# Performance work log

Hardware: AMD Instinct MI355X
Metric: run time of the kernel (lower is better)

The kernel has to match this reference:

```python
import jax, jax.numpy as jnp
import numpy as np

NUM_HEADS = 8
HEAD_SPLITS = [2, 3, 3]            # heads per crpe window {3:2, 5:3, 7:3}
WINDOWS = [3, 5, 7]


def dwconv(x, w, b, pad):
    """Depthwise conv. x: [B,C,H,W], w: [C,1,kh,kw] (OIHW), b: [C]."""
    y = jax.lax.conv_general_dilated(
        x, w, window_strides=(1, 1), padding=[(pad, pad), (pad, pad)],
        dimension_numbers=("NCHW", "OIHW", "NCHW"),
        feature_group_count=x.shape[1])
    return y + b[None, :, None, None]


def layernorm(x, w, b, eps=1e-6):
    m = jnp.mean(x, axis=-1, keepdims=True)
    v = jnp.mean(jnp.square(x - m), axis=-1, keepdims=True)
    return (x - m) * jax.lax.rsqrt(v + eps) * w + b


def setup_inputs() -> dict:
    key = jax.random.key(0)
    ks = jax.random.split(key, 16)
    B, Hs, Ws, C = 16, 56, 56, 512
    N = Hs * Ws
    Ch = C // NUM_HEADS
    hid = int(C * 4.0)

    def rn(k, shape, s=0.02):
        return jax.random.normal(k, shape, jnp.float32) * s

    return {
        "x": jax.random.normal(ks[0], (B, N, C), jnp.float32),
        "H": Hs, "W": Ws,
        "cpe_w": rn(ks[1], (C, 1, 3, 3)), "cpe_b": jnp.zeros((C,), jnp.float32),
        "ln1_w": jnp.ones((C,), jnp.float32), "ln1_b": jnp.zeros((C,), jnp.float32),
        "qkv_w": rn(ks[2], (C, 3 * C)),
        "proj_w": rn(ks[3], (C, C)), "proj_b": jnp.zeros((C,), jnp.float32),
        "w3": rn(ks[4], (HEAD_SPLITS[0] * Ch, 1, 3, 3)), "b3": jnp.zeros((HEAD_SPLITS[0] * Ch,), jnp.float32),
        "w5": rn(ks[5], (HEAD_SPLITS[1] * Ch, 1, 5, 5)), "b5": jnp.zeros((HEAD_SPLITS[1] * Ch,), jnp.float32),
        "w7": rn(ks[6], (HEAD_SPLITS[2] * Ch, 1, 7, 7)), "b7": jnp.zeros((HEAD_SPLITS[2] * Ch,), jnp.float32),
        "ln2_w": jnp.ones((C,), jnp.float32), "ln2_b": jnp.zeros((C,), jnp.float32),
        "fc1_w": rn(ks[7], (C, hid)), "fc1_b": jnp.zeros((hid,), jnp.float32),
        "fc2_w": rn(ks[8], (hid, C)), "fc2_b": jnp.zeros((C,), jnp.float32),
    }


def reference(x, H, W, cpe_w, cpe_b, ln1_w, ln1_b, qkv_w, proj_w, proj_b,
              w3, b3, w5, b5, w7, b7, ln2_w, ln2_b, fc1_w, fc1_b, fc2_w, fc2_b):
    B, N, C = x.shape
    h = NUM_HEADS
    Ch = C // h
    scale = Ch ** -0.5

    # --- ConvPosEnc (no cls token: N == H*W branch) ---
    feat = jnp.transpose(x, (0, 2, 1)).reshape(B, C, H, W)
    feat = dwconv(feat, cpe_w, cpe_b, pad=1) + feat
    x0 = jnp.transpose(feat.reshape(B, C, N), (0, 2, 1))  # [B,N,C]

    # --- FactorAttnConvRelPosEnc ---
    cur = layernorm(x0, ln1_w, ln1_b)
    qkv = (cur @ qkv_w).reshape(B, N, 3, h, Ch)
    qkv = jnp.transpose(qkv, (2, 0, 3, 1, 4))  # [3,B,h,N,Ch]
    q, k, v = qkv[0], qkv[1], qkv[2]

    k_sm = jax.nn.softmax(k, axis=2)                    # softmax over tokens
    kv = jnp.einsum("bhnk,bhnv->bhkv", k_sm, v)         # [B,h,Ch,Ch]
    factor_att = jnp.einsum("bhnk,bhkv->bhnv", q, kv)   # [B,h,N,Ch]

    # ConvRelPosEnc: grouped depthwise convs on v per head split
    v_img = jnp.transpose(v, (0, 1, 3, 2)).reshape(B, h * Ch, H, W)
    c0, c1 = HEAD_SPLITS[0] * Ch, (HEAD_SPLITS[0] + HEAD_SPLITS[1]) * Ch
    conv_v = jnp.concatenate([
        dwconv(v_img[:, :c0], w3, b3, pad=1),
        dwconv(v_img[:, c0:c1], w5, b5, pad=2),
        dwconv(v_img[:, c1:], w7, b7, pad=3),
    ], axis=1)
    conv_v = jnp.transpose(conv_v.reshape(B, h, Ch, N), (0, 1, 3, 2))  # [B,h,N,Ch]
    crpe = q * conv_v

    attn = scale * factor_att + crpe
    attn = jnp.transpose(attn, (0, 2, 1, 3)).reshape(B, N, C)
    attn = attn @ proj_w + proj_b

    x0 = x0 + attn

    # --- FFN ---
    cur = layernorm(x0, ln2_w, ln2_b)
    hdn = jax.nn.gelu(cur @ fc1_w + fc1_b, approximate=False)
    out = x0 + (hdn @ fc2_w + fc2_b)
    return out
```

## Files before the change

### kernel.cpp

```cpp
#include <hip/hip_runtime.h>
#include <hip/hip_bf16.h>

typedef unsigned short ushort_t;
typedef unsigned int uint_t;

typedef float f32x4 __attribute__((ext_vector_type(4)));
typedef short s16x8 __attribute__((ext_vector_type(8)));

#define HW 56
#define NTOK 3136
#define CDIM 512
#define NHEAD 8
#define CH 64
#define QKVC 1536
#define HID 2048
#define NSEG 28
#define SEGLEN 112

#define WPK_TOTAL 19976

__device__ __forceinline__ float b2f(ushort_t u) {
    union { uint_t i; float f; } cv; cv.i = ((uint_t)u) << 16; return cv.f;
}
__device__ __forceinline__ ushort_t f2b(float f) {
    union { __hip_bfloat16 h; ushort_t u; } cv; cv.h = __float2bfloat16(f); return cv.u;
}
__device__ __forceinline__ uint_t pk2(float a, float b) {
    return (uint_t)f2b(a) | ((uint_t)f2b(b) << 16);
}

__device__ __forceinline__ void gload_lds16(const ushort_t* g, ushort_t* l) {
    __builtin_amdgcn_global_load_lds(
        (const __attribute__((address_space(1))) void*)g,
        (__attribute__((address_space(3))) void*)l, 16, 0, 0);
}

__global__ __launch_bounds__(256) void k_transpose(const float* __restrict__ in,
                                                   ushort_t* __restrict__ out,
                                                   int K, int Npr) {
    __shared__ float tile[32][33];
    int tx = threadIdx.x & 31, ty = threadIdx.x >> 5;
    int kb = blockIdx.y * 32, nb = blockIdx.x * 32;
#pragma unroll
    for (int i = 0; i < 4; i++)
        tile[ty + i * 8][tx] = in[(size_t)(kb + ty + i * 8) * Npr + nb + tx];
    __syncthreads();
#pragma unroll
    for (int i = 0; i < 4; i++)
        out[(size_t)(nb + ty + i * 8) * K + kb + tx] = f2b(tile[tx][ty + i * 8]);
}

__global__ __launch_bounds__(256) void k_wtrans(const float* __restrict__ cpe_w,
                                                const float* __restrict__ w3,
                                                const float* __restrict__ w5,
                                                const float* __restrict__ w7,
                                                float* __restrict__ wpk) {
    int idx = blockIdx.x * 256 + threadIdx.x;
    if (idx < 4608) {
        int i = idx / 512, c = idx % 512;
        wpk[idx] = cpe_w[c * 9 + i];
    } else if (idx < 5760) {
        int r = idx - 4608; int i = r / 128, c = r % 128;
        wpk[idx] = w3[c * 9 + i];
    } else if (idx < 10560) {
        int r = idx - 5760; int i = r / 192, c = r % 192;
        wpk[idx] = w5[c * 25 + i];
    } else if (idx < 19968) {
        int r = idx - 10560; int i = r / 192, c = r % 192;
        wpk[idx] = w7[c * 49 + i];
    } else if (idx < WPK_TOTAL) {
        wpk[idx] = 0.f;
    }
}

__global__ __launch_bounds__(256) void k_cpe(const float* __restrict__ x,
                                             const float* __restrict__ wpk,
                                             const float* __restrict__ bias,
                                             float* __restrict__ x0) {
    int t = threadIdx.x;
    int tok = t >> 7;
    int c0 = (t & 127) * 4;
    int bb = blockIdx.y;
    int n = blockIdx.x * 2 + tok;
    int y = n / HW, xx = n % HW;
    const float* xb = x + ((size_t)bb * NTOK) * CDIM + c0;
    const float* zf = wpk + 19968;
    float4 a = *(const float4*)(bias + c0);
#pragma unroll
    for (int i = 0; i < 9; i++) {
        int ky = i / 3 - 1, kx = i % 3 - 1;
        int yy = y + ky, xc = xx + kx;
        bool ok = (unsigned)yy < HW && (unsigned)xc < HW;
        const float* ap = ok ? (xb + (size_t)(yy * HW + xc) * CDIM) : zf;
        float4 d = *(const float4*)ap;
        float4 w = *(const float4*)(wpk + i * 512 + c0);
        a.x += w.x * d.x; a.y += w.y * d.y; a.z += w.z * d.z; a.w += w.w * d.w;
    }
    float4 ctr = *(const float4*)(xb + (size_t)n * CDIM);
    a.x += ctr.x; a.y += ctr.y; a.z += ctr.z; a.w += ctr.w;
    *(float4*)(x0 + ((size_t)bb * NTOK + n) * CDIM + c0) = a;
}

__global__ __launch_bounds__(256) void k_ln(const float* __restrict__ in,
                                            const float* __restrict__ w,
                                            const float* __restrict__ b,
                                            ushort_t* __restrict__ out) {
    int wid = threadIdx.x >> 6, lane = threadIdx.x & 63;
    size_t row = (size_t)blockIdx.x * 4 + wid;
    const float* p = in + row * CDIM + lane * 8;
    float4 v0 = *(const float4*)p;
    float4 v1 = *(const float4*)(p + 4);
    float v[8] = { v0.x, v0.y, v0.z, v0.w, v1.x, v1.y, v1.z, v1.w };
    float s = 0.f, s2 = 0.f;
#pragma unroll
    for (int i = 0; i < 8; i++) { s += v[i]; s2 += v[i] * v[i]; }
#pragma unroll
    for (int m = 1; m < 64; m <<= 1) { s += __shfl_xor(s, m); s2 += __shfl_xor(s2, m); }
    float mean = s * (1.f / CDIM);
    float var = s2 * (1.f / CDIM) - mean * mean;
    float rstd = rsqrtf(var + 1e-6f);
    float4 w0 = *(const float4*)(w + lane * 8);
    float4 w1 = *(const float4*)(w + lane * 8 + 4);
    float4 b0 = *(const float4*)(b + lane * 8);
    float4 b1 = *(const float4*)(b + lane * 8 + 4);
    float wv[8] = { w0.x, w0.y, w0.z, w0.w, w1.x, w1.y, w1.z, w1.w };
    float bv[8] = { b0.x, b0.y, b0.z, b0.w, b1.x, b1.y, b1.z, b1.w };
    float o[8];
#pragma unroll
    for (int i = 0; i < 8; i++) o[i] = (v[i] - mean) * rstd * wv[i] + bv[i];
    uint4 ro;
    ro.x = pk2(o[0], o[1]); ro.y = pk2(o[2], o[3]); ro.z = pk2(o[4], o[5]); ro.w = pk2(o[6], o[7]);
    *(uint4*)(out + row * CDIM + lane * 8) = ro;
}

template <int EPI>
__global__ __launch_bounds__(256, 3) void k_gemm(const ushort_t* __restrict__ A,
                                                 const ushort_t* __restrict__ Bt,
                                                 const float* __restrict__ bias,
                                                 const float* __restrict__ res,
                                                 void* __restrict__ outv,
                                                 int M, int Npr, int K) {
    __shared__ ushort_t As[128 * 64];
    __shared__ ushort_t Bs[128 * 64];
    int t = threadIdx.x;
    int m0 = blockIdx.y * 128, n0 = blockIdx.x * 128;
    int wid = t >> 6, lane = t & 63, q = lane >> 4, r16 = lane & 15;
    int wr = wid >> 1, wc = wid & 1;
    f32x4 acc[4][4] = {};

    int srow = lane >> 3;
    int scol = ((lane & 7) ^ srow) * 8;
    const ushort_t* pA[4];
    const ushort_t* pB[4];
    int lofs[4];
#pragma unroll
    for (int c = 0; c < 4; c++) {
        int rowc = wid * 32 + c * 8 + srow;
        int ra = m0 + rowc; if (ra > M - 1) ra = M - 1;
        pA[c] = A + (size_t)ra * K + scol;
        pB[c] = Bt + (size_t)(n0 + rowc) * K + scol;
        lofs[c] = (wid * 32 + c * 8) * 64;
    }

    for (int k0 = 0; k0 < K; k0 += 64) {
#pragma unroll
        for (int c = 0; c < 4; c++) gload_lds16(pA[c] + k0, &As[lofs[c]]);
#pragma unroll
        for (int c = 0; c < 4; c++) gload_lds16(pB[c] + k0, &Bs[lofs[c]]);
        __syncthreads();
#pragma unroll
        for (int kk = 0; kk < 64; kk += 32) {
            s16x8 a[4], b[4];
#pragma unroll
            for (int i = 0; i < 4; i++) {
                int R = wr * 64 + i * 16 + r16;
                a[i] = *(const s16x8*)&As[R * 64 + ((kk + q * 8) ^ ((R & 7) * 8))];
            }
#pragma unroll
            for (int j = 0; j < 4; j++) {
                int S = wc * 64 + j * 16 + r16;
                b[j] = *(const s16x8*)&Bs[S * 64 + ((kk + q * 8) ^ ((S & 7) * 8))];
            }
#pragma unroll
            for (int mi = 0; mi < 4; mi++)
#pragma unroll
                for (int ni = 0; ni < 4; ni++)
                    acc[mi][ni] = __builtin_amdgcn_mfma_f32_16x16x32_bf16(a[mi], b[ni], acc[mi][ni], 0, 0, 0);
        }
        __syncthreads();
    }

#pragma unroll
    for (int mi = 0; mi < 4; mi++) {
#pragma unroll
        for (int ni = 0; ni < 4; ni++) {
            int col = n0 + wc * 64 + ni * 16 + r16;
            float bv = 0.f;
            if (EPI != 0) bv = bias[col];
#pragma unroll
            for (int r = 0; r < 4; r++) {
                int row = m0 + wr * 64 + mi * 16 + q * 4 + r;
                if (row >= M) continue;
                float xv = acc[mi][ni][r];
                size_t idx = (size_t)row * Npr + col;
                if (EPI == 0) {
                    ((ushort_t*)outv)[idx] = f2b(xv);
                } else if (EPI == 1) {
                    ((float*)outv)[idx] = xv + bv + res[idx];
                } else {
                    xv += bv;
                    xv = 0.5f * xv * (1.f + erff(xv * 0.70710678118654752f));
                    ((ushort_t*)outv)[idx] = f2b(xv);
                }
            }
        }
    }
}

__global__ __launch_bounds__(256) void k_sm_part(const ushort_t* __restrict__ qkv,
                                                 float* __restrict__ mxp,
                                                 float* __restrict__ ssp) {
    int cblk = blockIdx.x, seg = blockIdx.y, b = blockIdx.z;
    int ch = threadIdx.x & 63, nt = threadIdx.x >> 6;
    int c0 = cblk * 64;
    const ushort_t* base = qkv + (size_t)b * NTOK * QKVC + CDIM + c0 + ch;
    int nbeg = seg * SEGLEN, nend = nbeg + SEGLEN;
    __shared__ float red[4][64];
    float mx = -1e30f;
    for (int n = nbeg + nt; n < nend; n += 4) mx = fmaxf(mx, b2f(base[(size_t)n * QKVC]));
    red[nt][ch] = mx;
    __syncthreads();
    mx = fmaxf(fmaxf(red[0][ch], red[1][ch]), fmaxf(red[2][ch], red[3][ch]));
    __syncthreads();
    float s = 0.f;
    for (int n = nbeg + nt; n < nend; n += 4) s += __expf(b2f(base[(size_t)n * QKVC]) - mx);
    red[nt][ch] = s;
    __syncthreads();
    if (nt == 0) {
        s = red[0][ch] + red[1][ch] + red[2][ch] + red[3][ch];
        size_t o = ((size_t)b * CDIM + c0 + ch) * NSEG + seg;
        mxp[o] = mx;
        ssp[o] = s;
    }
}

__global__ __launch_bounds__(512) void k_sm_red(const float* __restrict__ mxp,
                                                const float* __restrict__ ssp,
                                                float* __restrict__ Mx,
                                                float* __restrict__ Sx) {
    int b = blockIdx.x, c = threadIdx.x;
    const float* mp = mxp + ((size_t)b * CDIM + c) * NSEG;
    const float* sp = ssp + ((size_t)b * CDIM + c) * NSEG;
    float m = -1e30f;
#pragma unroll 4
    for (int s = 0; s < NSEG; s++) m = fmaxf(m, mp[s]);
    float S = 0.f;
#pragma unroll 4
    for (int s = 0; s < NSEG; s++) S += sp[s] * __expf(mp[s] - m);
    Mx[b * CDIM + c] = m;
    Sx[b * CDIM + c] = S;
}

__global__ __launch_bounds__(256) void k_kv_part(const ushort_t* __restrict__ qkv,
                                                 const float* __restrict__ Mx,
                                                 float* __restrict__ kvpart) {
    int hd = blockIdx.x, seg = blockIdx.y, b = blockIdx.z;
    int c0 = hd * CH;
    int t = threadIdx.x, tx = t & 15, ty = t >> 4;
    __shared__ float mx[64];
    __shared__ float ek[8][64];
    __shared__ float vv[8][64];
    if (t < 64) mx[t] = Mx[b * CDIM + c0 + t];
    __syncthreads();
    float acc[4][4] = {};
    const ushort_t* kbase = qkv + (size_t)b * NTOK * QKVC + CDIM + c0;
    const ushort_t* vbase = kbase + CDIM;
    int nbeg = seg * SEGLEN;
    for (int n0 = nbeg; n0 < nbeg + SEGLEN; n0 += 8) {
        for (int idx = t; idx < 512; idx += 256) {
            int r = idx >> 6, ch = idx & 63;
            ek[r][ch] = __expf(b2f(kbase[(size_t)(n0 + r) * QKVC + ch]) - mx[ch]);
            vv[r][ch] = b2f(vbase[(size_t)(n0 + r) * QKVC + ch]);
        }
        __syncthreads();
#pragma unroll
        for (int r = 0; r < 8; r++) {
            float ekv[4], vvv[4];
#pragma unroll
            for (int i = 0; i < 4; i++) ekv[i] = ek[r][ty * 4 + i];
#pragma unroll
            for (int j = 0; j < 4; j++) vvv[j] = vv[r][tx * 4 + j];
#pragma unroll
            for (int i = 0; i < 4; i++)
#pragma unroll
                for (int j = 0; j < 4; j++) acc[i][j] += ekv[i] * vvv[j];
        }
        __syncthreads();
    }
    float* outp = kvpart + (((size_t)(b * NHEAD + hd)) * NSEG + seg) * 4096;
#pragma unroll
    for (int i = 0; i < 4; i++)
#pragma unroll
        for (int j = 0; j < 4; j++)
            outp[(size_t)(ty * 4 + i) * CH + tx * 4 + j] = acc[i][j];
}

__global__ __launch_bounds__(256) void k_kv_red(const float* __restrict__ kvpart,
                                                const float* __restrict__ Sx,
                                                float* __restrict__ kv) {
    int quad = blockIdx.x, hd = blockIdx.y, b = blockIdx.z;
    int bh = b * NHEAD + hd;
    int t = threadIdx.x;
    const float* basep = kvpart + ((size_t)bh * NSEG) * 4096 + quad * 1024;
    const float scale = 0.125f;
#pragma unroll
    for (int k = 0; k < 4; k++) {
        int e = k * 256 + t;
        float s = 0.f;
        for (int sg = 0; sg < NSEG; sg++) s += basep[(size_t)sg * 4096 + e];
        int ck = (quad * 1024 + e) >> 6;
        float sinv = scale / Sx[b * CDIM + hd * CH + ck];
        kv[(size_t)bh * 4096 + quad * 1024 + e] = s * sinv;
    }
}

__global__ __launch_bounds__(256) void k_convv(const ushort_t* __restrict__ qkv,
                                               const float* __restrict__ wpk,
                                               const float* __restrict__ b3,
                                               const float* __restrict__ b5,
                                               const float* __restrict__ b7,
                                               ushort_t* __restrict__ conv) {
    int t = threadIdx.x;
    int wv = t >> 6, lane = t & 63;
    int bb = blockIdx.y;
    int n0 = blockIdx.x * 16 + wv * 4;
    int ch0 = lane * 8;
    int ks, pad, base, stride; const float* bias;
    if (lane < 16)      { ks = 3; pad = 1; base = 4608 + ch0;          stride = 128; bias = b3 + ch0; }
    else if (lane < 40) { ks = 5; pad = 2; base = 5760 + (ch0 - 128);  stride = 192; bias = b5 + (ch0 - 128); }
    else                { ks = 7; pad = 3; base = 10560 + (ch0 - 320); stride = 192; bias = b7 + (ch0 - 320); }
    int ks2 = ks * ks;
    const ushort_t* vb = qkv + (size_t)bb * NTOK * QKVC + 2 * CDIM + ch0;
    const ushort_t* zp = (const ushort_t*)(wpk + 19968);
    float4 blo = *(const float4*)(bias);
    float4 bhi = *(const float4*)(bias + 4);
    float acc[4][8];
    int ty[4], txx[4];
#pragma unroll
    for (int k4 = 0; k4 < 4; k4++) {
        int n = n0 + k4; ty[k4] = n / HW; txx[k4] = n % HW;
        acc[k4][0] = blo.x; acc[k4][1] = blo.y; acc[k4][2] = blo.z; acc[k4][3] = blo.w;
        acc[k4][4] = bhi.x; acc[k4][5] = bhi.y; acc[k4][6] = bhi.z; acc[k4][7] = bhi.w;
    }
    int ky = -pad, kx = -pad;
    for (int i = 0; i < 49; i++) {
        bool act = i < ks2;
        int ie = act ? i : 0;
        const float* wp = wpk + base + ie * stride;
        float4 wlo = *(const float4*)wp;
        float4 whi = *(const float4*)(wp + 4);
        float w[8] = { wlo.x, wlo.y, wlo.z, wlo.w, whi.x, whi.y, whi.z, whi.w };
#pragma unroll
        for (int k4 = 0; k4 < 4; k4++) {
            int yy = ty[k4] + ky, xc = txx[k4] + kx;
            bool ok = act && (unsigned)yy < HW && (unsigned)xc < HW;
            const ushort_t* ap = ok ? (vb + (size_t)(yy * HW + xc) * QKVC) : zp;
            uint4 d = *(const uint4*)ap;
            float dv[8];
            dv[0] = b2f(d.x & 0xffff); dv[1] = b2f(d.x >> 16);
            dv[2] = b2f(d.y & 0xffff); dv[3] = b2f(d.y >> 16);
            dv[4] = b2f(d.z & 0xffff); dv[5] = b2f(d.z >> 16);
            dv[6] = b2f(d.w & 0xffff); dv[7] = b2f(d.w >> 16);
#pragma unroll
            for (int j = 0; j < 8; j++) acc[k4][j] += w[j] * dv[j];
        }
        kx++; if (kx > pad) { kx = -pad; ky++; }
    }
#pragma unroll
    for (int k4 = 0; k4 < 4; k4++) {
        int n = n0 + k4;
        uint4 o;
        o.x = pk2(acc[k4][0], acc[k4][1]);
        o.y = pk2(acc[k4][2], acc[k4][3]);
        o.z = pk2(acc[k4][4], acc[k4][5]);
        o.w = pk2(acc[k4][6], acc[k4][7]);
        *(uint4*)&conv[((size_t)bb * NTOK + n) * CDIM + ch0] = o;
    }
}

__global__ __launch_bounds__(256) void k_attn(const ushort_t* __restrict__ qkv,
                                              const float* __restrict__ kv,
                                              ushort_t* __restrict__ conv) {
    int nb = blockIdx.x, hd = blockIdx.y, b = blockIdx.z;
    int t = threadIdx.x, tx = t & 15, ty = t >> 4;
    __shared__ float kvl[64 * 64];
    __shared__ float ql[64 * 65];
    const float* kvsrc = kv + (size_t)(b * NHEAD + hd) * CH * CH;
    for (int idx = t; idx < 4096; idx += 256) kvl[idx] = kvsrc[idx];
    const ushort_t* qbase = qkv + ((size_t)b * NTOK + nb * 64) * QKVC + hd * CH;
    for (int idx = t; idx < 4096; idx += 256) {
        int r = idx >> 6, ck = idx & 63;
        ql[r * 65 + ck] = b2f(qbase[(size_t)r * QKVC + ck]);
    }
    __syncthreads();
    float acc[4][4] = {};
    for (int ck = 0; ck < 64; ck++) {
        float kvr[4];
#pragma unroll
        for (int j = 0; j < 4; j++) kvr[j] = kvl[ck * 64 + tx * 4 + j];
#pragma unroll
        for (int i = 0; i < 4; i++) {
            float qv = ql[(ty + 16 * i) * 65 + ck];
#pragma unroll
            for (int j = 0; j < 4; j++) acc[i][j] += qv * kvr[j];
        }
    }
    size_t obase = (size_t)b * NTOK + nb * 64;
#pragma unroll
    for (int i = 0; i < 4; i++) {
        int row = ty + 16 * i;
        size_t o = (obase + row) * CDIM + hd * CH + tx * 4;
        uint2 cv = *(const uint2*)&conv[o];
        float c0 = b2f((ushort_t)(cv.x & 0xffff)), c1 = b2f((ushort_t)(cv.x >> 16));
        float c2 = b2f((ushort_t)(cv.y & 0xffff)), c3 = b2f((ushort_t)(cv.y >> 16));
        float q0 = ql[row * 65 + tx * 4 + 0];
        float q1 = ql[row * 65 + tx * 4 + 1];
        float q2 = ql[row * 65 + tx * 4 + 2];
        float q3 = ql[row * 65 + tx * 4 + 3];
        uint2 ov;
        ov.x = pk2(acc[i][0] + q0 * c0, acc[i][1] + q1 * c1);
        ov.y = pk2(acc[i][2] + q2 * c2, acc[i][3] + q3 * c3);
        *(uint2*)&conv[o] = ov;
    }
}

extern "C" void kernel_launch(void* const* d_in, const int* in_sizes, int n_in,
                              void* d_out, int out_size, void* d_ws, size_t ws_size,
                              hipStream_t stream) {
    const float* x     = (const float*)d_in[0];
    const float* cpe_w = (const float*)d_in[3];
    const float* cpe_b = (const float*)d_in[4];
    const float* ln1_w = (const float*)d_in[5];
    const float* ln1_b = (const float*)d_in[6];
    const float* qkv_w = (const float*)d_in[7];
    const float* proj_w = (const float*)d_in[8];
    const float* proj_b = (const float*)d_in[9];
    const float* w3 = (const float*)d_in[10];
    const float* b3 = (const float*)d_in[11];
    const float* w5 = (const float*)d_in[12];
    const float* b5 = (const float*)d_in[13];
    const float* w7 = (const float*)d_in[14];
    const float* b7 = (const float*)d_in[15];
    const float* ln2_w = (const float*)d_in[16];
    const float* ln2_b = (const float*)d_in[17];
    const float* fc1_w = (const float*)d_in[18];
    const float* fc1_b = (const float*)d_in[19];
    const float* fc2_w = (const float*)d_in[20];
    const float* fc2_b = (const float*)d_in[21];
    float* out = (float*)d_out;

    char* p = (char*)d_ws;
    ushort_t* wt_qkv  = (ushort_t*)p; p += (size_t)QKVC * CDIM * 2;
    ushort_t* wt_proj = (ushort_t*)p; p += (size_t)CDIM * CDIM * 2;
    ushort_t* wt_fc1  = (ushort_t*)p; p += (size_t)HID * CDIM * 2;
    ushort_t* wt_fc2  = (ushort_t*)p; p += (size_t)CDIM * HID * 2;
    float* wpk = (float*)p; p += 20480 * 4;
    size_t wt_bytes = (size_t)(p - (char*)d_ws);

    k_transpose<<<dim3(QKVC / 32, CDIM / 32), 256, 0, stream>>>(qkv_w, wt_qkv, CDIM, QKVC);
    k_transpose<<<dim3(CDIM / 32, CDIM / 32), 256, 0, stream>>>(proj_w, wt_proj, CDIM, CDIM);
    k_transpose<<<dim3(HID / 32, CDIM / 32), 256, 0, stream>>>(fc1_w, wt_fc1, CDIM, HID);
    k_transpose<<<dim3(CDIM / 32, HID / 32), 256, 0, stream>>>(fc2_w, wt_fc2, HID, CDIM);
    k_wtrans<<<(WPK_TOTAL + 255) / 256, 256, 0, stream>>>(cpe_w, w3, w5, w7, wpk);

    const size_t per_b = (size_t)NTOK * CDIM * 2
                       + (size_t)NTOK * HID * 2
                       + (size_t)NHEAD * CH * CH * 4
                       + (size_t)NHEAD * NSEG * 4096 * 4
                       + (size_t)CDIM * 4 * 2
                       + (size_t)CDIM * NSEG * 4 * 2;
    int Bc = 16;
    while (Bc > 1 && wt_bytes + (size_t)Bc * per_b > ws_size) Bc >>= 1;

    ushort_t* cur = (ushort_t*)p; p += (size_t)Bc * NTOK * CDIM * 2;
    char* un = p;                 p += (size_t)Bc * NTOK * HID * 2;
    ushort_t* conv = (ushort_t*)un;
    ushort_t* qkvb = (ushort_t*)(un + (size_t)Bc * NTOK * CDIM * 2);
    ushort_t* hid  = (ushort_t*)un;
    float* kvb    = (float*)p; p += (size_t)Bc * NHEAD * CH * CH * 4;
    float* kvpart = (float*)p; p += (size_t)Bc * NHEAD * NSEG * 4096 * 4;
    float* Mx  = (float*)p; p += (size_t)Bc * CDIM * 4;
    float* Sx  = (float*)p; p += (size_t)Bc * CDIM * 4;
    float* mxp = (float*)p; p += (size_t)Bc * CDIM * NSEG * 4;
    float* ssp = (float*)p;

    for (int b0 = 0; b0 < 16; b0 += Bc) {
        int M = Bc * NTOK;
        int gy = (M + 127) / 128;
        const float* xch = x + (size_t)b0 * NTOK * CDIM;
        float* och = out + (size_t)b0 * NTOK * CDIM;
        float* x0 = och;

        k_cpe<<<dim3(NTOK / 2, Bc), 256, 0, stream>>>(xch, wpk, cpe_b, x0);
        k_ln<<<M / 4, 256, 0, stream>>>(x0, ln1_w, ln1_b, cur);
        k_gemm<0><<<dim3(QKVC / 128, gy), 256, 0, stream>>>(cur, wt_qkv, nullptr, nullptr, qkvb, M, QKVC, CDIM);
        k_sm_part<<<dim3(8, NSEG, Bc), 256, 0, stream>>>(qkvb, mxp, ssp);
        k_sm_red<<<Bc, 512, 0, stream>>>(mxp, ssp, Mx, Sx);
        k_kv_part<<<dim3(NHEAD, NSEG, Bc), 256, 0, stream>>>(qkvb, Mx, kvpart);
        k_kv_red<<<dim3(4, NHEAD, Bc), 256, 0, stream>>>(kvpart, Sx, kvb);
        k_convv<<<dim3(NTOK / 16, Bc), 256, 0, stream>>>(qkvb, wpk, b3, b5, b7, conv);
        k_attn<<<dim3(NTOK / 64, NHEAD, Bc), 256, 0, stream>>>(qkvb, kvb, conv);
        k_gemm<1><<<dim3(CDIM / 128, gy), 256, 0, stream>>>(conv, wt_proj, proj_b, x0, x0, M, CDIM, CDIM);
        k_ln<<<M / 4, 256, 0, stream>>>(x0, ln2_w, ln2_b, cur);
        k_gemm<2><<<dim3(HID / 128, gy), 256, 0, stream>>>(cur, wt_fc1, fc1_b, nullptr, hid, M, HID, CDIM);
        k_gemm<1><<<dim3(CDIM / 128, gy), 256, 0, stream>>>(hid, wt_fc2, fc2_b, x0, och, M, CDIM, HID);
    }
}
```

Measured before the change: 1.271 ms.

## Fuse CPE with LayerNorm, swizzle GEMM blocks, online softmax stats, split conv kernels

```diff
diff --git a/kernel.cpp b/kernel.cpp
--- a/kernel.cpp
+++ b/kernel.cpp
@@ -73,13 +73,17 @@
     }
 }
 
-__global__ __launch_bounds__(256) void k_cpe(const float* __restrict__ x,
-                                             const float* __restrict__ wpk,
-                                             const float* __restrict__ bias,
-                                             float* __restrict__ x0) {
+__global__ __launch_bounds__(256) void k_cpe_ln(const float* __restrict__ x,
+                                                const float* __restrict__ wpk,
+                                                const float* __restrict__ bias,
+                                                const float* __restrict__ lnw,
+                                                const float* __restrict__ lnb,
+                                                float* __restrict__ x0,
+                                                ushort_t* __restrict__ cur) {
     int t = threadIdx.x;
     int tok = t >> 7;
-    int c0 = (t & 127) * 4;
+    int tl = t & 127;
+    int c0 = tl * 4;
     int bb = blockIdx.y;
     int n = blockIdx.x * 2 + tok;
     int y = n / HW, xx = n % HW;
@@ -99,6 +103,28 @@
     float4 ctr = *(const float4*)(xb + (size_t)n * CDIM);
     a.x += ctr.x; a.y += ctr.y; a.z += ctr.z; a.w += ctr.w;
     *(float4*)(x0 + ((size_t)bb * NTOK + n) * CDIM + c0) = a;
+
+    float s = a.x + a.y + a.z + a.w;
+    float s2 = a.x * a.x + a.y * a.y + a.z * a.z + a.w * a.w;
+#pragma unroll
+    for (int m = 1; m < 64; m <<= 1) { s += __shfl_xor(s, m); s2 += __shfl_xor(s2, m); }
+    __shared__ float rs[4], rs2[4];
+    int wid = t >> 6, lane = t & 63;
+    if (lane == 0) { rs[wid] = s; rs2[wid] = s2; }
+    __syncthreads();
+    s = rs[tok * 2] + rs[tok * 2 + 1];
+    s2 = rs2[tok * 2] + rs2[tok * 2 + 1];
+    float mean = s * (1.f / CDIM);
+    float var = s2 * (1.f / CDIM) - mean * mean;
+    float rstd = rsqrtf(var + 1e-6f);
+    float4 wv = *(const float4*)(lnw + c0);
+    float4 bv = *(const float4*)(lnb + c0);
+    float o0 = (a.x - mean) * rstd * wv.x + bv.x;
+    float o1 = (a.y - mean) * rstd * wv.y + bv.y;
+    float o2 = (a.z - mean) * rstd * wv.z + bv.z;
+    float o3 = (a.w - mean) * rstd * wv.w + bv.w;
+    uint2 ro; ro.x = pk2(o0, o1); ro.y = pk2(o2, o3);
+    *(uint2*)(cur + ((size_t)bb * NTOK + n) * CDIM + c0) = ro;
 }
 
 __global__ __launch_bounds__(256) void k_ln(const float* __restrict__ in,
@@ -143,7 +169,18 @@
     __shared__ ushort_t As[128 * 64];
     __shared__ ushort_t Bs[128 * 64];
     int t = threadIdx.x;
-    int m0 = blockIdx.y * 128, n0 = blockIdx.x * 128;
+
+    int gx = gridDim.x;
+    int bx = blockIdx.x, by = blockIdx.y;
+    int nwg = gx * gridDim.y;
+    if ((nwg & 7) == 0) {
+        int fid = by * gx + bx;
+        int cpx = nwg >> 3;
+        int swz = (fid & 7) * cpx + (fid >> 3);
+        bx = swz % gx; by = swz / gx;
+    }
+    int m0 = by * 128, n0 = bx * 128;
+
     int wid = t >> 6, lane = t & 63, q = lane >> 4, r16 = lane & 15;
     int wr = wid >> 1, wc = wid & 1;
     f32x4 acc[4][4] = {};
@@ -225,22 +262,26 @@
     int c0 = cblk * 64;
     const ushort_t* base = qkv + (size_t)b * NTOK * QKVC + CDIM + c0 + ch;
     int nbeg = seg * SEGLEN, nend = nbeg + SEGLEN;
-    __shared__ float red[4][64];
-    float mx = -1e30f;
-    for (int n = nbeg + nt; n < nend; n += 4) mx = fmaxf(mx, b2f(base[(size_t)n * QKVC]));
-    red[nt][ch] = mx;
-    __syncthreads();
-    mx = fmaxf(fmaxf(red[0][ch], red[1][ch]), fmaxf(red[2][ch], red[3][ch]));
-    __syncthreads();
-    float s = 0.f;
-    for (int n = nbeg + nt; n < nend; n += 4) s += __expf(b2f(base[(size_t)n * QKVC]) - mx);
-    red[nt][ch] = s;
+    __shared__ float redm[4][64], reds[4][64];
+    float mx = -1e30f, sum = 0.f;
+    for (int n = nbeg + nt; n < nend; n += 4) {
+        float v = b2f(base[(size_t)n * QKVC]);
+        float mn = fmaxf(mx, v);
+        sum = sum * __expf(mx - mn) + __expf(v - mn);
+        mx = mn;
+    }
+    redm[nt][ch] = mx;
+    reds[nt][ch] = sum;
     __syncthreads();
     if (nt == 0) {
-        s = red[0][ch] + red[1][ch] + red[2][ch] + red[3][ch];
+        float m = fmaxf(fmaxf(redm[0][ch], redm[1][ch]), fmaxf(redm[2][ch], redm[3][ch]));
+        float S = reds[0][ch] * __expf(redm[0][ch] - m)
+                + reds[1][ch] * __expf(redm[1][ch] - m)
+                + reds[2][ch] * __expf(redm[2][ch] - m)
+                + reds[3][ch] * __expf(redm[3][ch] - m);
         size_t o = ((size_t)b * CDIM + c0 + ch) * NSEG + seg;
-        mxp[o] = mx;
-        ssp[o] = s;
+        mxp[o] = m;
+        ssp[o] = S;
     }
 }
 
@@ -324,68 +365,53 @@
     }
 }
 
-__global__ __launch_bounds__(256) void k_convv(const ushort_t* __restrict__ qkv,
-                                               const float* __restrict__ wpk,
-                                               const float* __restrict__ b3,
-                                               const float* __restrict__ b5,
-                                               const float* __restrict__ b7,
-                                               ushort_t* __restrict__ conv) {
+template <int KS>
+__global__ __launch_bounds__(KS == 3 ? 256 : 192) void k_conv(const ushort_t* __restrict__ qkv,
+                                                              const float* __restrict__ wpk,
+                                                              const float* __restrict__ bias,
+                                                              ushort_t* __restrict__ conv) {
+    constexpr int PAD = KS / 2;
+    constexpr int CHBASE = (KS == 3) ? 0 : ((KS == 5) ? 128 : 320);
+    constexpr int WBASE = (KS == 3) ? 4608 : ((KS == 5) ? 5760 : 10560);
+    constexpr int WSTR = (KS == 3) ? 128 : 192;
+    constexpr int GRP = (KS == 3) ? 16 : 24;
+    constexpr int TOKB = (KS == 3) ? 16 : 8;
     int t = threadIdx.x;
-    int wv = t >> 6, lane = t & 63;
     int bb = blockIdx.y;
-    int n0 = blockIdx.x * 16 + wv * 4;
-    int ch0 = lane * 8;
-    int ks, pad, base, stride; const float* bias;
-    if (lane < 16)      { ks = 3; pad = 1; base = 4608 + ch0;          stride = 128; bias = b3 + ch0; }
-    else if (lane < 40) { ks = 5; pad = 2; base = 5760 + (ch0 - 128);  stride = 192; bias = b5 + (ch0 - 128); }
-    else                { ks = 7; pad = 3; base = 10560 + (ch0 - 320); stride = 192; bias = b7 + (ch0 - 320); }
-    int ks2 = ks * ks;
-    const ushort_t* vb = qkv + (size_t)bb * NTOK * QKVC + 2 * CDIM + ch0;
+    int n = blockIdx.x * TOKB + t / GRP;
+    int g = t % GRP;
+    int crel = g * 8;
+    int y = n / HW, xx = n % HW;
+    const ushort_t* vb = qkv + (size_t)bb * NTOK * QKVC + 2 * CDIM + CHBASE + crel;
     const ushort_t* zp = (const ushort_t*)(wpk + 19968);
-    float4 blo = *(const float4*)(bias);
-    float4 bhi = *(const float4*)(bias + 4);
-    float acc[4][8];
-    int ty[4], txx[4];
-#pragma unroll
-    for (int k4 = 0; k4 < 4; k4++) {
-        int n = n0 + k4; ty[k4] = n / HW; txx[k4] = n % HW;
-        acc[k4][0] = blo.x; acc[k4][1] = blo.y; acc[k4][2] = blo.z; acc[k4][3] = blo.w;
-        acc[k4][4] = bhi.x; acc[k4][5] = bhi.y; acc[k4][6] = bhi.z; acc[k4][7] = bhi.w;
-    }
-    int ky = -pad, kx = -pad;
-    for (int i = 0; i < 49; i++) {
-        bool act = i < ks2;
-        int ie = act ? i : 0;
-        const float* wp = wpk + base + ie * stride;
+    float4 blo = *(const float4*)(bias + crel);
+    float4 bhi = *(const float4*)(bias + crel + 4);
+    float acc[8] = { blo.x, blo.y, blo.z, blo.w, bhi.x, bhi.y, bhi.z, bhi.w };
+#pragma unroll
+    for (int i = 0; i < KS * KS; i++) {
+        int ky = i / KS - PAD, kx = i % KS - PAD;
+        int yy = y + ky, xc = xx + kx;
+        bool ok = (unsigned)yy < HW && (unsigned)xc < HW;
+        const ushort_t* ap = ok ? (vb + (size_t)(yy * HW + xc) * QKVC) : zp;
+        uint4 d = *(const uint4*)ap;
+        const float* wp = wpk + WBASE + i * WSTR + crel;
         float4 wlo = *(const float4*)wp;
         float4 whi = *(const float4*)(wp + 4);
-        float w[8] = { wlo.x, wlo.y, wlo.z, wlo.w, whi.x, whi.y, whi.z, whi.w };
-#pragma unroll
-        for (int k4 = 0; k4 < 4; k4++) {
-            int yy = ty[k4] + ky, xc = txx[k4] + kx;
-            bool ok = act && (unsigned)yy < HW && (unsigned)xc < HW;
-            const ushort_t* ap = ok ? (vb + (size_t)(yy * HW + xc) * QKVC) : zp;
-            uint4 d = *(const uint4*)ap;
-            float dv[8];
-            dv[0] = b2f(d.x & 0xffff); dv[1] = b2f(d.x >> 16);
-            dv[2] = b2f(d.y & 0xffff); dv[3] = b2f(d.y >> 16);
-            dv[4] = b2f(d.z & 0xffff); dv[5] = b2f(d.z >> 16);
-            dv[6] = b2f(d.w & 0xffff); dv[7] = b2f(d.w >> 16);
-#pragma unroll
-            for (int j = 0; j < 8; j++) acc[k4][j] += w[j] * dv[j];
-        }
-        kx++; if (kx > pad) { kx = -pad; ky++; }
-    }
-#pragma unroll
-    for (int k4 = 0; k4 < 4; k4++) {
-        int n = n0 + k4;
-        uint4 o;
-        o.x = pk2(acc[k4][0], acc[k4][1]);
-        o.y = pk2(acc[k4][2], acc[k4][3]);
-        o.z = pk2(acc[k4][4], acc[k4][5]);
-        o.w = pk2(acc[k4][6], acc[k4][7]);
-        *(uint4*)&conv[((size_t)bb * NTOK + n) * CDIM + ch0] = o;
-    }
+        acc[0] += wlo.x * b2f((ushort_t)(d.x & 0xffff));
+        acc[1] += wlo.y * b2f((ushort_t)(d.x >> 16));
+        acc[2] += wlo.z * b2f((ushort_t)(d.y & 0xffff));
+        acc[3] += wlo.w * b2f((ushort_t)(d.y >> 16));
+        acc[4] += whi.x * b2f((ushort_t)(d.z & 0xffff));
+        acc[5] += whi.y * b2f((ushort_t)(d.z >> 16));
+        acc[6] += whi.z * b2f((ushort_t)(d.w & 0xffff));
+        acc[7] += whi.w * b2f((ushort_t)(d.w >> 16));
+    }
+    uint4 o;
+    o.x = pk2(acc[0], acc[1]);
+    o.y = pk2(acc[2], acc[3]);
+    o.z = pk2(acc[4], acc[5]);
+    o.w = pk2(acc[6], acc[7]);
+    *(uint4*)&conv[((size_t)bb * NTOK + n) * CDIM + CHBASE + crel] = o;
 }
 
 __global__ __launch_bounds__(256) void k_attn(const ushort_t* __restrict__ qkv,
@@ -501,14 +527,15 @@
         float* och = out + (size_t)b0 * NTOK * CDIM;
         float* x0 = och;
 
-        k_cpe<<<dim3(NTOK / 2, Bc), 256, 0, stream>>>(xch, wpk, cpe_b, x0);
-        k_ln<<<M / 4, 256, 0, stream>>>(x0, ln1_w, ln1_b, cur);
+        k_cpe_ln<<<dim3(NTOK / 2, Bc), 256, 0, stream>>>(xch, wpk, cpe_b, ln1_w, ln1_b, x0, cur);
         k_gemm<0><<<dim3(QKVC / 128, gy), 256, 0, stream>>>(cur, wt_qkv, nullptr, nullptr, qkvb, M, QKVC, CDIM);
         k_sm_part<<<dim3(8, NSEG, Bc), 256, 0, stream>>>(qkvb, mxp, ssp);
         k_sm_red<<<Bc, 512, 0, stream>>>(mxp, ssp, Mx, Sx);
         k_kv_part<<<dim3(NHEAD, NSEG, Bc), 256, 0, stream>>>(qkvb, Mx, kvpart);
         k_kv_red<<<dim3(4, NHEAD, Bc), 256, 0, stream>>>(kvpart, Sx, kvb);
-        k_convv<<<dim3(NTOK / 16, Bc), 256, 0, stream>>>(qkvb, wpk, b3, b5, b7, conv);
+        k_conv<3><<<dim3(NTOK / 16, Bc), 256, 0, stream>>>(qkvb, wpk, b3, conv);
+        k_conv<5><<<dim3(NTOK / 8, Bc), 192, 0, stream>>>(qkvb, wpk, b5, conv);
+        k_conv<7><<<dim3(NTOK / 8, Bc), 192, 0, stream>>>(qkvb, wpk, b7, conv);
         k_attn<<<dim3(NTOK / 64, NHEAD, Bc), 256, 0, stream>>>(qkvb, kvb, conv);
         k_gemm<1><<<dim3(CDIM / 128, gy), 256, 0, stream>>>(conv, wt_proj, proj_b, x0, x0, M, CDIM, CDIM);
         k_ln<<<M / 4, 256, 0, stream>>>(x0, ln2_w, ln2_b, cur);
```

New measurement: 1.493 ms. 17.4% more time.
